# Kernel tuning notes

Hardware: AMD Instinct MI355X
Metric: run time of the kernel (lower is better)

Reference implementation:

```python
import jax, jax.numpy as jnp
import numpy as np

TOP_K = 4


def setup_inputs() -> dict:
    key = jax.random.key(0)
    ks = jax.random.split(key, 8)
    B, S, D, I, E = 4, 2048, 1024, 512, 16
    scale = 0.05  # keep activations numerically sane (torch init uses raw randn)
    return {
        "x": jax.random.normal(ks[0], (B, S, D), dtype=jnp.float32),
        "router_w": jax.random.normal(ks[1], (E, D), dtype=jnp.float32) * scale,
        "w1_w": jax.random.normal(ks[2], (E, I, D), dtype=jnp.float32) * scale,
        "w1_b": jax.random.normal(ks[3], (E, I), dtype=jnp.float32) * scale,
        "w2_w": jax.random.normal(ks[4], (E, D, I), dtype=jnp.float32) * scale,
        "w2_b": jax.random.normal(ks[5], (E, D), dtype=jnp.float32) * scale,
        "w3_w": jax.random.normal(ks[6], (E, I, D), dtype=jnp.float32) * scale,
        "w3_b": jax.random.normal(ks[7], (E, I), dtype=jnp.float32) * scale,
    }


def reference(x, router_w, w1_w, w1_b, w2_w, w2_b, w3_w, w3_b):
    B, S, D = x.shape
    E = router_w.shape[0]
    K = TOP_K
    # router: softmax over experts, then top-k
    scores = jax.nn.softmax(jnp.einsum('bsd,ed->bse', x, router_w), axis=-1)
    top_scores, sel = jax.lax.top_k(scores, K)            # [B,S,K]
    sel_flat = sel.reshape(B, S * K)                      # flattened expert ids
    ts_flat = top_scores.reshape(B, S * K)
    # stable argsort by expert id -> dispatch order
    idxs = jnp.argsort(sel_flat, axis=-1, stable=True)    # [B, S*K]
    ts = jnp.take_along_axis(ts_flat, idxs, axis=-1)      # [B, S*K]
    tok = idxs // K                                       # source token index
    # gather tokens into dispatch order
    xs = jnp.take_along_axis(x, tok[:, :, None], axis=1)  # [B, S*K, D]
    T = (S * K) // E                                      # tokens per expert (fixed)
    xs = xs.reshape(B, E, T, D).transpose(1, 0, 2, 3).reshape(E, B * T, D)
    h1 = jnp.einsum('end,eid->eni', xs, w1_w) + w1_b[:, None, :]
    h3 = jnp.einsum('end,eid->eni', xs, w3_w) + w3_b[:, None, :]
    h = jax.nn.silu(h1) * h3
    out = jnp.einsum('eni,edi->end', h, w2_w) + w2_b[:, None, :]  # [E, B*T, D]
    # un-permute back to [B, S*K, D], weight by router scores
    out = out.reshape(E, B, T, D).transpose(1, 0, 2, 3).reshape(B, S * K, D)
    out = out * ts[:, :, None]
    # scatter-add combine back to token positions
    res = jax.vmap(lambda t, o: jnp.zeros((S, D), x.dtype).at[t].add(o))(tok, out)
    return res
```

## Files before the change

kernel.cpp:

```cpp
#include <hip/hip_runtime.h>

typedef _Float16 f16;
typedef f16 f16x8 __attribute__((ext_vector_type(8)));
typedef float f32x4 __attribute__((ext_vector_type(4)));

#define B_ 4
#define S_ 2048
#define D_ 1024
#define I_ 512
#define E_ 16
#define K_ 4
#define TPB_ 8192
#define EROWS_ 2048

__device__ __forceinline__ void gload16(const void* g, void* l) {
    __builtin_amdgcn_global_load_lds(
        (const __attribute__((address_space(1))) void*)g,
        (__attribute__((address_space(3))) void*)l, 16, 0, 0);
}

__device__ __forceinline__ int xcd_swz(int bid, int nwg) {
    int cpx = nwg >> 3;
    return (bid & 7) * cpx + (bid >> 3);
}

__device__ __forceinline__ void cvt8(const float* __restrict__ s, f16* __restrict__ d, int i) {
    const float4* sp = (const float4*)s;
    float4 a = sp[2 * i], b = sp[2 * i + 1];
    f16x8 v;
    v[0] = (f16)a.x; v[1] = (f16)a.y; v[2] = (f16)a.z; v[3] = (f16)a.w;
    v[4] = (f16)b.x; v[5] = (f16)b.y; v[6] = (f16)b.z; v[7] = (f16)b.w;
    *(f16x8*)(d + (size_t)i * 8) = v;
}

__global__ void k_convert(const float* __restrict__ x, const float* __restrict__ w1,
                          const float* __restrict__ w3, const float* __restrict__ w2,
                          f16* __restrict__ xh, f16* __restrict__ w1h,
                          f16* __restrict__ w3h, f16* __restrict__ w2h) {
    const int N8 = (B_ * S_ * D_) / 8;
    int stride = gridDim.x * blockDim.x;
    for (int i = blockIdx.x * blockDim.x + threadIdx.x; i < N8; i += stride) {
        cvt8(x, xh, i);
        cvt8(w1, w1h, i);
        cvt8(w3, w3h, i);
        cvt8(w2, w2h, i);
    }
}

__global__ void k_router(const float* __restrict__ x, const float* __restrict__ rw,
                         int* __restrict__ sel, float* __restrict__ ts) {
    int w = threadIdx.x >> 6, lane = threadIdx.x & 63;
    int tok = blockIdx.x * 4 + w;
    const float4* xp = (const float4*)(x + (size_t)tok * D_);
    float xr[16];
    #pragma unroll
    for (int j = 0; j < 4; ++j) {
        float4 v = xp[lane * 4 + j];
        xr[j * 4 + 0] = v.x; xr[j * 4 + 1] = v.y; xr[j * 4 + 2] = v.z; xr[j * 4 + 3] = v.w;
    }
    float sc[E_];
    #pragma unroll
    for (int e = 0; e < E_; ++e) {
        const float4* wp = (const float4*)(rw + (size_t)e * D_);
        float a = 0.f;
        #pragma unroll
        for (int j = 0; j < 4; ++j) {
            float4 v = wp[lane * 4 + j];
            a += xr[j * 4 + 0] * v.x + xr[j * 4 + 1] * v.y + xr[j * 4 + 2] * v.z + xr[j * 4 + 3] * v.w;
        }
        #pragma unroll
        for (int off = 32; off; off >>= 1) a += __shfl_xor(a, off);
        sc[e] = a;
    }
    float mx = sc[0];
    #pragma unroll
    for (int e = 1; e < E_; ++e) mx = fmaxf(mx, sc[e]);
    float ex[E_]; float sum = 0.f;
    #pragma unroll
    for (int e = 0; e < E_; ++e) { ex[e] = __expf(sc[e] - mx); sum += ex[e]; }
    float inv = 1.f / sum;
    if (lane == 0) {
        unsigned usedMask = 0;
        #pragma unroll
        for (int k = 0; k < K_; ++k) {
            int bi = -1; float bv = -1e30f, bev = 0.f;
            #pragma unroll
            for (int e = 0; e < E_; ++e) {
                bool ok = !((usedMask >> e) & 1) && (sc[e] > bv);
                if (ok) { bv = sc[e]; bi = e; bev = ex[e]; }
            }
            usedMask |= 1u << bi;
            sel[(size_t)tok * K_ + k] = bi;
            ts[(size_t)tok * K_ + k] = bev * inv;
        }
    }
}

__global__ void k_sort(const int* __restrict__ sel, int* __restrict__ src_tok,
                       int* __restrict__ invp) {
    __shared__ int ssel[TPB_];
    __shared__ int scnt[E_];
    int b = blockIdx.x, tid = threadIdx.x;
    for (int i = 0; i < 8; ++i) ssel[i * 1024 + tid] = sel[(size_t)b * TPB_ + i * 1024 + tid];
    __syncthreads();
    int e = tid >> 6, lane = tid & 63;
    unsigned long long lm = (1ull << lane) - 1ull;
    int c = 0;
    for (int ch = 0; ch < 128; ++ch) {
        unsigned long long m = __ballot(ssel[ch * 64 + lane] == e);
        c += __popcll(m);
    }
    if (lane == 0) scnt[e] = c;
    __syncthreads();
    int run = 0;
    for (int i = 0; i < E_; ++i) run += (i < e) ? scnt[i] : 0;
    for (int ch = 0; ch < 128; ++ch) {
        int f = ch * 64 + lane;
        int s = ssel[f];
        unsigned long long m = __ballot(s == e);
        if (s == e) {
            int p = run + __popcll(m & lm);
            src_tok[(size_t)b * TPB_ + p] = f >> 2;
            invp[(size_t)b * TPB_ + f] = p;
        }
        run += __popcll(m);
    }
}

__global__ __launch_bounds__(256, 2) void k_gemm1(
    const f16* __restrict__ xh, const f16* __restrict__ w1h, const f16* __restrict__ w3h,
    const float* __restrict__ b1, const float* __restrict__ b3,
    const int* __restrict__ src_tok, f16* __restrict__ h) {
    __shared__ f16 Als[128 * 64];
    __shared__ f16 B1s[128 * 64];
    __shared__ f16 B3s[128 * 64];
    int bid = xcd_swz(blockIdx.x, 1024);
    int e = bid >> 6, rem = bid & 63, mb = rem >> 2, nb = rem & 3;
    int tid = threadIdx.x, lane = tid & 63, w = tid >> 6, wr = w >> 1, wc = w & 1;

    int lr = lane >> 3;
    int cswz = (lane & 7) ^ lr;
    const f16* arow[4];
    int bofs[4];
    int ldsA[4];
    #pragma unroll
    for (int i = 0; i < 4; ++i) {
        int r = w * 32 + i * 8 + lr;
        int re = mb * 128 + r;
        int bb = re >> 9;
        int tokk = src_tok[bb * TPB_ + e * 512 + (re & 511)];
        arow[i] = xh + ((size_t)(bb * S_ + tokk)) * D_ + cswz * 8;
        int brw = nb * 128 + r;
        bofs[i] = (e * I_ + brw) * D_ + cswz * 8;
        ldsA[i] = w * 2048 + i * 512;
    }

    f32x4 acc1[4][4], acc3[4][4];
    const f32x4 fz = {0.f, 0.f, 0.f, 0.f};
    #pragma unroll
    for (int m = 0; m < 4; ++m)
        #pragma unroll
        for (int n = 0; n < 4; ++n) { acc1[m][n] = fz; acc3[m][n] = fz; }

    for (int ks = 0; ks < 16; ++ks) {
        __syncthreads();
        int ko = ks * 64;
        #pragma unroll
        for (int i = 0; i < 4; ++i) {
            gload16(arow[i] + ko, &Als[ldsA[i]]);
            gload16(w1h + bofs[i] + ko, &B1s[ldsA[i]]);
            gload16(w3h + bofs[i] + ko, &B3s[ldsA[i]]);
        }
        __syncthreads();
        #pragma unroll
        for (int kk = 0; kk < 2; ++kk) {
            f16x8 af[4], bf1[4], bf3[4];
            int kb = kk * 32 + (lane >> 4) * 8;
            #pragma unroll
            for (int m = 0; m < 4; ++m) {
                int row = wr * 64 + m * 16 + (lane & 15);
                af[m] = *(const f16x8*)&Als[row * 64 + (kb ^ ((row & 7) * 8))];
            }
            #pragma unroll
            for (int n = 0; n < 4; ++n) {
                int row = wc * 64 + n * 16 + (lane & 15);
                int o = row * 64 + (kb ^ ((row & 7) * 8));
                bf1[n] = *(const f16x8*)&B1s[o];
                bf3[n] = *(const f16x8*)&B3s[o];
            }
            #pragma unroll
            for (int m = 0; m < 4; ++m)
                #pragma unroll
                for (int n = 0; n < 4; ++n) {
                    acc1[m][n] = __builtin_amdgcn_mfma_f32_16x16x32_f16(af[m], bf1[n], acc1[m][n], 0, 0, 0);
                    acc3[m][n] = __builtin_amdgcn_mfma_f32_16x16x32_f16(af[m], bf3[n], acc3[m][n], 0, 0, 0);
                }
        }
    }
    int icb = nb * 128 + wc * 64;
    float bias1[4], bias3[4];
    #pragma unroll
    for (int n = 0; n < 4; ++n) {
        int ic = icb + n * 16 + (lane & 15);
        bias1[n] = b1[e * I_ + ic];
        bias3[n] = b3[e * I_ + ic];
    }
    #pragma unroll
    for (int m = 0; m < 4; ++m)
        #pragma unroll
        for (int n = 0; n < 4; ++n) {
            int col = icb + n * 16 + (lane & 15);
            #pragma unroll
            for (int r = 0; r < 4; ++r) {
                float z1 = acc1[m][n][r] + bias1[n];
                float z3 = acc3[m][n][r] + bias3[n];
                float sv = z1 / (1.f + __expf(-z1));
                float hv = sv * z3;
                int row = mb * 128 + wr * 64 + m * 16 + (lane >> 4) * 4 + r;
                h[((size_t)e * EROWS_ + row) * I_ + col] = (f16)hv;
            }
        }
}

__global__ __launch_bounds__(256, 2) void k_gemm2(
    const f16* __restrict__ h, const f16* __restrict__ w2h, const float* __restrict__ b2,
    f16* __restrict__ h2p) {
    __shared__ f16 Als[128 * 64];
    __shared__ f16 Bs[128 * 64];
    int bid = xcd_swz(blockIdx.x, 2048);
    int e = bid >> 7, rem = bid & 127, mb = rem >> 3, nb = rem & 7;
    int tid = threadIdx.x, lane = tid & 63, w = tid >> 6, wr = w >> 1, wc = w & 1;

    int lr = lane >> 3;
    int cswz = (lane & 7) ^ lr;
    size_t aofs[4], bofs[4];
    int ldsA[4];
    #pragma unroll
    for (int i = 0; i < 4; ++i) {
        int r = w * 32 + i * 8 + lr;
        aofs[i] = ((size_t)e * EROWS_ + mb * 128 + r) * I_ + cswz * 8;
        bofs[i] = ((size_t)e * D_ + nb * 128 + r) * I_ + cswz * 8;
        ldsA[i] = w * 2048 + i * 512;
    }

    f32x4 acc[4][4];
    const f32x4 fz = {0.f, 0.f, 0.f, 0.f};
    #pragma unroll
    for (int m = 0; m < 4; ++m)
        #pragma unroll
        for (int n = 0; n < 4; ++n) acc[m][n] = fz;

    for (int ks = 0; ks < 8; ++ks) {
        __syncthreads();
        int ko = ks * 64;
        #pragma unroll
        for (int i = 0; i < 4; ++i) {
            gload16(h + aofs[i] + ko, &Als[ldsA[i]]);
            gload16(w2h + bofs[i] + ko, &Bs[ldsA[i]]);
        }
        __syncthreads();
        #pragma unroll
        for (int kk = 0; kk < 2; ++kk) {
            f16x8 af[4], bf[4];
            int kb = kk * 32 + (lane >> 4) * 8;
            #pragma unroll
            for (int m = 0; m < 4; ++m) {
                int row = wr * 64 + m * 16 + (lane & 15);
                af[m] = *(const f16x8*)&Als[row * 64 + (kb ^ ((row & 7) * 8))];
            }
            #pragma unroll
            for (int n = 0; n < 4; ++n) {
                int row = wc * 64 + n * 16 + (lane & 15);
                bf[n] = *(const f16x8*)&Bs[row * 64 + (kb ^ ((row & 7) * 8))];
            }
            #pragma unroll
            for (int m = 0; m < 4; ++m)
                #pragma unroll
                for (int n = 0; n < 4; ++n)
                    acc[m][n] = __builtin_amdgcn_mfma_f32_16x16x32_f16(af[m], bf[n], acc[m][n], 0, 0, 0);
        }
    }
    int dcb = nb * 128 + wc * 64;
    float bias[4];
    #pragma unroll
    for (int n = 0; n < 4; ++n) bias[n] = b2[e * D_ + dcb + n * 16 + (lane & 15)];
    #pragma unroll
    for (int m = 0; m < 4; ++m)
        #pragma unroll
        for (int r = 0; r < 4; ++r) {
            int row = mb * 128 + wr * 64 + m * 16 + (lane >> 4) * 4 + r;
            #pragma unroll
            for (int n = 0; n < 4; ++n) {
                int col = dcb + n * 16 + (lane & 15);
                h2p[((size_t)e * EROWS_ + row) * D_ + col] = (f16)(acc[m][n][r] + bias[n]);
            }
        }
}

__global__ __launch_bounds__(256, 2) void k_gemm2_atomic(
    const f16* __restrict__ h, const f16* __restrict__ w2h, const float* __restrict__ b2,
    const int* __restrict__ src_tok, const int* __restrict__ invp,
    const float* __restrict__ ts, float* __restrict__ out) {
    __shared__ f16 Als[128 * 64];
    __shared__ f16 Bs[128 * 64];
    int bid = xcd_swz(blockIdx.x, 2048);
    int e = bid >> 7, rem = bid & 127, mb = rem >> 3, nb = rem & 7;
    int tid = threadIdx.x, lane = tid & 63, w = tid >> 6, wr = w >> 1, wc = w & 1;

    int lr = lane >> 3;
    int cswz = (lane & 7) ^ lr;
    size_t aofs[4], bofs[4];
    int ldsA[4];
    #pragma unroll
    for (int i = 0; i < 4; ++i) {
        int r = w * 32 + i * 8 + lr;
        aofs[i] = ((size_t)e * EROWS_ + mb * 128 + r) * I_ + cswz * 8;
        bofs[i] = ((size_t)e * D_ + nb * 128 + r) * I_ + cswz * 8;
        ldsA[i] = w * 2048 + i * 512;
    }
    f32x4 acc[4][4];
    const f32x4 fz = {0.f, 0.f, 0.f, 0.f};
    #pragma unroll
    for (int m = 0; m < 4; ++m)
        #pragma unroll
        for (int n = 0; n < 4; ++n) acc[m][n] = fz;
    for (int ks = 0; ks < 8; ++ks) {
        __syncthreads();
        int ko = ks * 64;
        #pragma unroll
        for (int i = 0; i < 4; ++i) {
            gload16(h + aofs[i] + ko, &Als[ldsA[i]]);
            gload16(w2h + bofs[i] + ko, &Bs[ldsA[i]]);
        }
        __syncthreads();
        #pragma unroll
        for (int kk = 0; kk < 2; ++kk) {
            f16x8 af[4], bf[4];
            int kb = kk * 32 + (lane >> 4) * 8;
            #pragma unroll
            for (int m = 0; m < 4; ++m) {
                int row = wr * 64 + m * 16 + (lane & 15);
                af[m] = *(const f16x8*)&Als[row * 64 + (kb ^ ((row & 7) * 8))];
            }
            #pragma unroll
            for (int n = 0; n < 4; ++n) {
                int row = wc * 64 + n * 16 + (lane & 15);
                bf[n] = *(const f16x8*)&Bs[row * 64 + (kb ^ ((row & 7) * 8))];
            }
            #pragma unroll
            for (int m = 0; m < 4; ++m)
                #pragma unroll
                for (int n = 0; n < 4; ++n)
                    acc[m][n] = __builtin_amdgcn_mfma_f32_16x16x32_f16(af[m], bf[n], acc[m][n], 0, 0, 0);
        }
    }
    int dcb = nb * 128 + wc * 64;
    float bias[4];
    #pragma unroll
    for (int n = 0; n < 4; ++n) bias[n] = b2[e * D_ + dcb + n * 16 + (lane & 15)];
    #pragma unroll
    for (int m = 0; m < 4; ++m)
        #pragma unroll
        for (int r = 0; r < 4; ++r) {
            int re = mb * 128 + wr * 64 + m * 16 + (lane >> 4) * 4 + r;
            int bb = re >> 9;
            int pos = bb * TPB_ + e * 512 + (re & 511);
            int tokk = src_tok[pos];
            float g = 0.f;
            #pragma unroll
            for (int k = 0; k < K_; ++k)
                if (invp[bb * TPB_ + tokk * K_ + k] == e * 512 + (re & 511))
                    g = ts[bb * TPB_ + tokk * K_ + k];
            float* op = out + ((size_t)(bb * S_ + tokk)) * D_;
            #pragma unroll
            for (int n = 0; n < 4; ++n) {
                int col = dcb + n * 16 + (lane & 15);
                atomicAdd(op + col, g * (acc[m][n][r] + bias[n]));
            }
        }
}

__global__ __launch_bounds__(256) void k_combine(
    const f16* __restrict__ h2p, const float* __restrict__ ts,
    const int* __restrict__ invp, float* __restrict__ out) {
    int w = threadIdx.x >> 6, lane = threadIdx.x & 63;
    int t = blockIdx.x * 4 + w;
    int b = t >> 11, s = t & 2047;
    int base = b * TPB_ + s * 4;
    float g[4]; const f16* rows[4];
    #pragma unroll
    for (int k = 0; k < 4; ++k) {
        int p = invp[base + k];
        g[k] = ts[base + k];
        int e = p >> 9, n = (b << 9) + (p & 511);
        rows[k] = h2p + ((size_t)(e * EROWS_ + n)) * D_;
    }
    float* op = out + (size_t)t * D_;
    #pragma unroll
    for (int c = 0; c < 2; ++c) {
        int d = c * 512 + lane * 8;
        float a[8] = {0.f};
        #pragma unroll
        for (int k = 0; k < 4; ++k) {
            f16x8 v = *(const f16x8*)(rows[k] + d);
            #pragma unroll
            for (int j = 0; j < 8; ++j) a[j] += g[k] * (float)v[j];
        }
        *(float4*)(op + d)     = make_float4(a[0], a[1], a[2], a[3]);
        *(float4*)(op + d + 4) = make_float4(a[4], a[5], a[6], a[7]);
    }
}

extern "C" void kernel_launch(void* const* d_in, const int* in_sizes, int n_in,
                              void* d_out, int out_size, void* d_ws, size_t ws_size,
                              hipStream_t stream) {
    const float* x  = (const float*)d_in[0];
    const float* rw = (const float*)d_in[1];
    const float* w1 = (const float*)d_in[2];
    const float* b1 = (const float*)d_in[3];
    const float* w2 = (const float*)d_in[4];
    const float* b2 = (const float*)d_in[5];
    const float* w3 = (const float*)d_in[6];
    const float* b3 = (const float*)d_in[7];
    float* out = (float*)d_out;

    const size_t NEL = (size_t)B_ * S_ * D_;
    char* p = (char*)d_ws;
    f16* xh  = (f16*)p; p += NEL * 2;
    f16* w1h = (f16*)p; p += NEL * 2;
    f16* w3h = (f16*)p; p += NEL * 2;
    f16* w2h = (f16*)p; p += NEL * 2;
    f16* h   = (f16*)p; p += (size_t)E_ * EROWS_ * I_ * 2;
    int*   sel     = (int*)p;   p += (size_t)B_ * TPB_ * 4;
    float* ts      = (float*)p; p += (size_t)B_ * TPB_ * 4;
    int*   src_tok = (int*)p;   p += (size_t)B_ * TPB_ * 4;
    int*   invp    = (int*)p;   p += (size_t)B_ * TPB_ * 4;
    f16* h2p = (f16*)p; p += (size_t)E_ * EROWS_ * D_ * 2;
    size_t need = (size_t)(p - (char*)d_ws);

    k_convert<<<2048, 256, 0, stream>>>(x, w1, w3, w2, xh, w1h, w3h, w2h);
    k_router<<<2048, 256, 0, stream>>>(x, rw, sel, ts);
    k_sort<<<4, 1024, 0, stream>>>(sel, src_tok, invp);
    k_gemm1<<<1024, 256, 0, stream>>>(xh, w1h, w3h, b1, b3, src_tok, h);
    if (ws_size >= need) {
        k_gemm2<<<2048, 256, 0, stream>>>(h, w2h, b2, h2p);
        k_combine<<<2048, 256, 0, stream>>>(h2p, ts, invp, out);
    } else {
        hipMemsetAsync(d_out, 0, (size_t)out_size * sizeof(float), stream);
        k_gemm2_atomic<<<2048, 256, 0, stream>>>(h, w2h, b2, src_tok, invp, ts, out);
    }
}
```

Measured before the change: 355.1 us.

## Double-buffer LDS in expert GEMMs and widen gemm1 tile to 256 rows

Both expert GEMM kernels now use two LDS buffers. The global_load_lds copy for the next K-slice is issued before computing the current slice, and s_waitcnt vmcnt(8) waits only for the older stage, so memory traffic overlaps with MFMA work. The fused w1/w3 GEMM also moves to 512-thread blocks that cover 256 token rows, halving the grid and reusing each weight tile across twice as many rows. The cost is far more LDS per block (about 128KB for gemm1), which allows only one block per CU and depends on exact manual vmcnt accounting.

```diff
diff --git a/kernel.cpp b/kernel.cpp
--- a/kernel.cpp
+++ b/kernel.cpp
@@ -127,32 +127,41 @@
     }
 }
 
-__global__ __launch_bounds__(256, 2) void k_gemm1(
+#define PIPE_WAIT8()  asm volatile("s_waitcnt vmcnt(8)" ::: "memory")
+#define PIPE_WAIT0()  asm volatile("s_waitcnt vmcnt(0)" ::: "memory")
+#define PIPE_BAR()    do { __builtin_amdgcn_s_barrier(); __builtin_amdgcn_sched_barrier(0); } while (0)
+#define PIPE_ENDBAR() do { __builtin_amdgcn_sched_barrier(0); __builtin_amdgcn_s_barrier(); } while (0)
+
+__global__ __launch_bounds__(512, 1) void k_gemm1(
     const f16* __restrict__ xh, const f16* __restrict__ w1h, const f16* __restrict__ w3h,
     const float* __restrict__ b1, const float* __restrict__ b3,
     const int* __restrict__ src_tok, f16* __restrict__ h) {
-    __shared__ f16 Als[128 * 64];
-    __shared__ f16 B1s[128 * 64];
-    __shared__ f16 B3s[128 * 64];
-    int bid = xcd_swz(blockIdx.x, 1024);
-    int e = bid >> 6, rem = bid & 63, mb = rem >> 2, nb = rem & 3;
+    __shared__ f16 Als[2][256 * 64];
+    __shared__ f16 B1s[2][128 * 64];
+    __shared__ f16 B3s[2][128 * 64];
+    int bid = xcd_swz(blockIdx.x, 512);
+    int e = bid >> 5, rem = bid & 31, mb = rem >> 2, nb = rem & 3;
     int tid = threadIdx.x, lane = tid & 63, w = tid >> 6, wr = w >> 1, wc = w & 1;
 
     int lr = lane >> 3;
     int cswz = (lane & 7) ^ lr;
     const f16* arow[4];
-    int bofs[4];
-    int ldsA[4];
+    int bofs[2];
+    int ldsA[4], ldsB[2];
     #pragma unroll
     for (int i = 0; i < 4; ++i) {
-        int r = w * 32 + i * 8 + lr;
-        int re = mb * 128 + r;
+        int r = i * 64 + w * 8 + lr;
+        int re = mb * 256 + r;
         int bb = re >> 9;
         int tokk = src_tok[bb * TPB_ + e * 512 + (re & 511)];
         arow[i] = xh + ((size_t)(bb * S_ + tokk)) * D_ + cswz * 8;
-        int brw = nb * 128 + r;
-        bofs[i] = (e * I_ + brw) * D_ + cswz * 8;
-        ldsA[i] = w * 2048 + i * 512;
+        ldsA[i] = (i * 64 + w * 8) * 64;
+    }
+    #pragma unroll
+    for (int i = 0; i < 2; ++i) {
+        int r = i * 64 + w * 8 + lr;
+        bofs[i] = (e * I_ + nb * 128 + r) * D_ + cswz * 8;
+        ldsB[i] = (i * 64 + w * 8) * 64;
     }
 
     f32x4 acc1[4][4], acc3[4][4];
@@ -162,41 +171,46 @@
         #pragma unroll
         for (int n = 0; n < 4; ++n) { acc1[m][n] = fz; acc3[m][n] = fz; }
 
-    for (int ks = 0; ks < 16; ++ks) {
-        __syncthreads();
-        int ko = ks * 64;
-        #pragma unroll
-        for (int i = 0; i < 4; ++i) {
-            gload16(arow[i] + ko, &Als[ldsA[i]]);
-            gload16(w1h + bofs[i] + ko, &B1s[ldsA[i]]);
-            gload16(w3h + bofs[i] + ko, &B3s[ldsA[i]]);
-        }
-        __syncthreads();
-        #pragma unroll
-        for (int kk = 0; kk < 2; ++kk) {
-            f16x8 af[4], bf1[4], bf3[4];
-            int kb = kk * 32 + (lane >> 4) * 8;
-            #pragma unroll
-            for (int m = 0; m < 4; ++m) {
-                int row = wr * 64 + m * 16 + (lane & 15);
-                af[m] = *(const f16x8*)&Als[row * 64 + (kb ^ ((row & 7) * 8))];
-            }
-            #pragma unroll
-            for (int n = 0; n < 4; ++n) {
-                int row = wc * 64 + n * 16 + (lane & 15);
-                int o = row * 64 + (kb ^ ((row & 7) * 8));
-                bf1[n] = *(const f16x8*)&B1s[o];
-                bf3[n] = *(const f16x8*)&B3s[o];
-            }
-            #pragma unroll
-            for (int m = 0; m < 4; ++m)
-                #pragma unroll
-                for (int n = 0; n < 4; ++n) {
-                    acc1[m][n] = __builtin_amdgcn_mfma_f32_16x16x32_f16(af[m], bf1[n], acc1[m][n], 0, 0, 0);
-                    acc3[m][n] = __builtin_amdgcn_mfma_f32_16x16x32_f16(af[m], bf3[n], acc3[m][n], 0, 0, 0);
-                }
-        }
-    }
+#define STAGE1(t, bsel) do { int ko_ = (t) * 64;                                   \
+    _Pragma("unroll") for (int i_ = 0; i_ < 4; ++i_)                               \
+        gload16(arow[i_] + ko_, &Als[bsel][ldsA[i_]]);                             \
+    _Pragma("unroll") for (int i_ = 0; i_ < 2; ++i_) {                             \
+        gload16(w1h + bofs[i_] + ko_, &B1s[bsel][ldsB[i_]]);                       \
+        gload16(w3h + bofs[i_] + ko_, &B3s[bsel][ldsB[i_]]); } } while (0)
+
+#define COMPUTE1(bsel)                                                             \
+    _Pragma("unroll") for (int kk = 0; kk < 2; ++kk) {                             \
+        f16x8 af[4], bf1[4], bf3[4];                                               \
+        int kb = kk * 32 + (lane >> 4) * 8;                                        \
+        _Pragma("unroll") for (int m = 0; m < 4; ++m) {                            \
+            int row = wr * 64 + m * 16 + (lane & 15);                              \
+            af[m] = *(const f16x8*)&Als[bsel][row * 64 + (kb ^ ((row & 7) * 8))];  \
+        }                                                                          \
+        _Pragma("unroll") for (int n = 0; n < 4; ++n) {                            \
+            int row = wc * 64 + n * 16 + (lane & 15);                              \
+            int o = row * 64 + (kb ^ ((row & 7) * 8));                             \
+            bf1[n] = *(const f16x8*)&B1s[bsel][o];                                 \
+            bf3[n] = *(const f16x8*)&B3s[bsel][o];                                 \
+        }                                                                          \
+        _Pragma("unroll") for (int m = 0; m < 4; ++m)                              \
+            _Pragma("unroll") for (int n = 0; n < 4; ++n) {                        \
+                acc1[m][n] = __builtin_amdgcn_mfma_f32_16x16x32_f16(af[m], bf1[n], acc1[m][n], 0, 0, 0); \
+                acc3[m][n] = __builtin_amdgcn_mfma_f32_16x16x32_f16(af[m], bf3[n], acc3[m][n], 0, 0, 0); \
+            }                                                                      \
+    }
+
+    STAGE1(0, 0);
+    for (int t = 0; t < 15; ++t) {
+        STAGE1(t + 1, (t + 1) & 1);
+        PIPE_WAIT8();
+        PIPE_BAR();
+        COMPUTE1(t & 1);
+        PIPE_ENDBAR();
+    }
+    PIPE_WAIT0();
+    PIPE_BAR();
+    COMPUTE1(1);
+
     int icb = nb * 128 + wc * 64;
     float bias1[4], bias3[4];
     #pragma unroll
@@ -216,17 +230,19 @@
                 float z3 = acc3[m][n][r] + bias3[n];
                 float sv = z1 / (1.f + __expf(-z1));
                 float hv = sv * z3;
-                int row = mb * 128 + wr * 64 + m * 16 + (lane >> 4) * 4 + r;
+                int row = mb * 256 + wr * 64 + m * 16 + (lane >> 4) * 4 + r;
                 h[((size_t)e * EROWS_ + row) * I_ + col] = (f16)hv;
             }
         }
+#undef STAGE1
+#undef COMPUTE1
 }
 
 __global__ __launch_bounds__(256, 2) void k_gemm2(
     const f16* __restrict__ h, const f16* __restrict__ w2h, const float* __restrict__ b2,
     f16* __restrict__ h2p) {
-    __shared__ f16 Als[128 * 64];
-    __shared__ f16 Bs[128 * 64];
+    __shared__ f16 Als[2][128 * 64];
+    __shared__ f16 Bs[2][128 * 64];
     int bid = xcd_swz(blockIdx.x, 2048);
     int e = bid >> 7, rem = bid & 127, mb = rem >> 3, nb = rem & 7;
     int tid = threadIdx.x, lane = tid & 63, w = tid >> 6, wr = w >> 1, wc = w & 1;
@@ -234,13 +250,13 @@
     int lr = lane >> 3;
     int cswz = (lane & 7) ^ lr;
     size_t aofs[4], bofs[4];
-    int ldsA[4];
+    int ldsO[4];
     #pragma unroll
     for (int i = 0; i < 4; ++i) {
         int r = w * 32 + i * 8 + lr;
         aofs[i] = ((size_t)e * EROWS_ + mb * 128 + r) * I_ + cswz * 8;
         bofs[i] = ((size_t)e * D_ + nb * 128 + r) * I_ + cswz * 8;
-        ldsA[i] = w * 2048 + i * 512;
+        ldsO[i] = w * 2048 + i * 512;
     }
 
     f32x4 acc[4][4];
@@ -250,36 +266,40 @@
         #pragma unroll
         for (int n = 0; n < 4; ++n) acc[m][n] = fz;
 
-    for (int ks = 0; ks < 8; ++ks) {
-        __syncthreads();
-        int ko = ks * 64;
-        #pragma unroll
-        for (int i = 0; i < 4; ++i) {
-            gload16(h + aofs[i] + ko, &Als[ldsA[i]]);
-            gload16(w2h + bofs[i] + ko, &Bs[ldsA[i]]);
-        }
-        __syncthreads();
-        #pragma unroll
-        for (int kk = 0; kk < 2; ++kk) {
-            f16x8 af[4], bf[4];
-            int kb = kk * 32 + (lane >> 4) * 8;
-            #pragma unroll
-            for (int m = 0; m < 4; ++m) {
-                int row = wr * 64 + m * 16 + (lane & 15);
-                af[m] = *(const f16x8*)&Als[row * 64 + (kb ^ ((row & 7) * 8))];
-            }
-            #pragma unroll
-            for (int n = 0; n < 4; ++n) {
-                int row = wc * 64 + n * 16 + (lane & 15);
-                bf[n] = *(const f16x8*)&Bs[row * 64 + (kb ^ ((row & 7) * 8))];
-            }
-            #pragma unroll
-            for (int m = 0; m < 4; ++m)
-                #pragma unroll
-                for (int n = 0; n < 4; ++n)
-                    acc[m][n] = __builtin_amdgcn_mfma_f32_16x16x32_f16(af[m], bf[n], acc[m][n], 0, 0, 0);
-        }
-    }
+#define STAGE2(t, bsel) do { int ko_ = (t) * 64;                                   \
+    _Pragma("unroll") for (int i_ = 0; i_ < 4; ++i_) {                             \
+        gload16(h + aofs[i_] + ko_, &Als[bsel][ldsO[i_]]);                         \
+        gload16(w2h + bofs[i_] + ko_, &Bs[bsel][ldsO[i_]]); } } while (0)
+
+#define COMPUTE2(bsel)                                                             \
+    _Pragma("unroll") for (int kk = 0; kk < 2; ++kk) {                             \
+        f16x8 af[4], bf[4];                                                        \
+        int kb = kk * 32 + (lane >> 4) * 8;                                        \
+        _Pragma("unroll") for (int m = 0; m < 4; ++m) {                            \
+            int row = wr * 64 + m * 16 + (lane & 15);                              \
+            af[m] = *(const f16x8*)&Als[bsel][row * 64 + (kb ^ ((row & 7) * 8))];  \
+        }                                                                          \
+        _Pragma("unroll") for (int n = 0; n < 4; ++n) {                            \
+            int row = wc * 64 + n * 16 + (lane & 15);                              \
+            bf[n] = *(const f16x8*)&Bs[bsel][row * 64 + (kb ^ ((row & 7) * 8))];   \
+        }                                                                          \
+        _Pragma("unroll") for (int m = 0; m < 4; ++m)                              \
+            _Pragma("unroll") for (int n = 0; n < 4; ++n)                          \
+                acc[m][n] = __builtin_amdgcn_mfma_f32_16x16x32_f16(af[m], bf[n], acc[m][n], 0, 0, 0); \
+    }
+
+    STAGE2(0, 0);
+    for (int t = 0; t < 7; ++t) {
+        STAGE2(t + 1, (t + 1) & 1);
+        PIPE_WAIT8();
+        PIPE_BAR();
+        COMPUTE2(t & 1);
+        PIPE_ENDBAR();
+    }
+    PIPE_WAIT0();
+    PIPE_BAR();
+    COMPUTE2(1);
+
     int dcb = nb * 128 + wc * 64;
     float bias[4];
     #pragma unroll
@@ -295,6 +315,8 @@
                 h2p[((size_t)e * EROWS_ + row) * D_ + col] = (f16)(acc[m][n][r] + bias[n]);
             }
         }
+#undef STAGE2
+#undef COMPUTE2
 }
 
 __global__ __launch_bounds__(256, 2) void k_gemm2_atomic(
@@ -441,7 +463,7 @@
     k_convert<<<2048, 256, 0, stream>>>(x, w1, w3, w2, xh, w1h, w3h, w2h);
     k_router<<<2048, 256, 0, stream>>>(x, rw, sel, ts);
     k_sort<<<4, 1024, 0, stream>>>(sel, src_tok, invp);
-    k_gemm1<<<1024, 256, 0, stream>>>(xh, w1h, w3h, b1, b3, src_tok, h);
+    k_gemm1<<<512, 512, 0, stream>>>(xh, w1h, w3h, b1, b3, src_tok, h);
     if (ws_size >= need) {
         k_gemm2<<<2048, 256, 0, stream>>>(h, w2h, b2, h2p);
         k_combine<<<2048, 256, 0, stream>>>(h2p, ts, invp, out);
```

After: 361.7 us. No clear change (+1.9%).
